# Kernel tuning notes

Measured on AMD Instinct MI355X. Metric: run time of the kernel, lower is better.

The kernel has to match this reference:

```python
import jax, jax.numpy as jnp
import numpy as np

B, N, E, H = 2, 4096, 512, 8
D = E // H  # head size


def setup_inputs() -> dict:
    key = jax.random.key(0)
    ks = jax.random.split(key, 11)
    s = 1.0 / np.sqrt(E)
    inp = {
        'q': jax.random.normal(ks[0], (B, N, E), jnp.float32),
        'k': jax.random.normal(ks[1], (B, N, E), jnp.float32),
        'v': jax.random.normal(ks[2], (B, N, E), jnp.float32),
        'Wq': jax.random.uniform(ks[3], (E, E), jnp.float32, -s, s),
        'bq': jax.random.uniform(ks[4], (E,), jnp.float32, -s, s),
        'Wk': jax.random.uniform(ks[5], (E, E), jnp.float32, -s, s),
        'bk': jax.random.uniform(ks[6], (E,), jnp.float32, -s, s),
        'Wv': jax.random.uniform(ks[7], (E, E), jnp.float32, -s, s),
        'bv': jax.random.uniform(ks[8], (E,), jnp.float32, -s, s),
        'Wo': jax.random.uniform(ks[9], (E, E), jnp.float32, -s, s),
        'bo': jax.random.uniform(ks[10], (E,), jnp.float32, -s, s),
    }
    return inp


def reference(q, k, v, Wq, bq, Wk, bk, Wv, bv, Wo, bo):
    # Linear projections (torch Linear: x @ W.T + b)
    qp = (q @ Wq.T + bq).reshape(B, N, H, D).transpose(0, 2, 1, 3)  # [B,H,N,D]
    kp = (k @ Wk.T + bk).reshape(B, N, H, D).transpose(0, 2, 1, 3)
    vp = (v @ Wv.T + bv).reshape(B, N, H, D).transpose(0, 2, 1, 3)
    scores = jnp.einsum('bhnd,bhmd->bhnm', qp, kp) / jnp.sqrt(jnp.float32(D))
    attn = jax.nn.softmax(scores, axis=-1)
    out = jnp.einsum('bhnm,bhmd->bhnd', attn, vp)  # [B,H,N,D]
    out = out.transpose(0, 2, 1, 3).reshape(B, N, E)
    return out @ Wo.T + bo
```

## Files before the change

kernel.cpp:

```cpp
#include <hip/hip_runtime.h>
#include <hip/hip_bf16.h>
#include <cstddef>
#include <cstdint>


typedef __bf16 bf16_t;
typedef __bf16 bf16x8 __attribute__((ext_vector_type(8)));
typedef __bf16 bf16x4 __attribute__((ext_vector_type(4)));
typedef float  f32x4  __attribute__((ext_vector_type(4)));

#define MFMA_BF16 __builtin_amdgcn_mfma_f32_16x16x32_bf16

static __device__ __forceinline__ bf16x8 cvt2(const float4& a, const float4& b) {
  return bf16x8{(bf16_t)a.x,(bf16_t)a.y,(bf16_t)a.z,(bf16_t)a.w,
                (bf16_t)b.x,(bf16_t)b.y,(bf16_t)b.z,(bf16_t)b.w};
}

static __device__ __forceinline__ uint32_t pk2(float a, float b) {
  uint32_t r;
  asm("v_cvt_pk_bf16_f32 %0, %1, %2" : "=v"(r) : "v"(a), "v"(b));
  return r;
}

__global__ void __launch_bounds__(256)
cvt_bf16(const float* __restrict__ q, const float* __restrict__ k,
         const float* __restrict__ v, const float* __restrict__ Wq,
         const float* __restrict__ Wk, const float* __restrict__ Wv,
         const float* __restrict__ Wo,
         bf16_t* __restrict__ qb, bf16_t* __restrict__ kb,
         bf16_t* __restrict__ vb, bf16_t* __restrict__ wq,
         bf16_t* __restrict__ wk, bf16_t* __restrict__ wv,
         bf16_t* __restrict__ wo)
{
  const int CQ = 524288;
  const int CW = 32768;
  const int TOT = 3 * CQ + 4 * CW;
  const int STRIDE = 2048 * 256;
  for (int c = blockIdx.x * 256 + threadIdx.x; c < TOT; c += STRIDE) {
    const float* src; bf16_t* dst; int off;
    if (c < 3 * CQ) {
      const int t = c >> 19;
      const int r = c & (CQ - 1);
      src = (t == 0) ? q : (t == 1) ? k : v;
      dst = (t == 0) ? qb : (t == 1) ? kb : vb;
      off = r << 3;
    } else {
      const int c2 = c - 3 * CQ;
      const int t = c2 >> 15;
      const int r = c2 & (CW - 1);
      src = (t == 0) ? Wq : (t == 1) ? Wk : (t == 2) ? Wv : Wo;
      dst = (t == 0) ? wq : (t == 1) ? wk : (t == 2) ? wv : wo;
      off = r << 3;
    }
    const float4 a = *(const float4*)(src + off);
    const float4 b = *(const float4*)(src + off + 4);
    *(bf16x8*)(dst + off) = cvt2(a, b);
  }
}

__global__ void __launch_bounds__(256, 3)
qkv_proj(const bf16_t* __restrict__ qb, const bf16_t* __restrict__ kb,
         const bf16_t* __restrict__ vb,
         const bf16_t* __restrict__ Wqb, const float* __restrict__ bq,
         const bf16_t* __restrict__ Wkb, const float* __restrict__ bk,
         const bf16_t* __restrict__ Wvb, const float* __restrict__ bv,
         bf16_t* __restrict__ Qp, bf16_t* __restrict__ Kp,
         bf16_t* __restrict__ Vt, float qscale)
{
  __shared__ __align__(16) bf16_t S[2 * 128 * 72];
  bf16_t* As = S;
  bf16_t* Bs = S + 128 * 72;

  const int l     = blockIdx.x;
  const int slice = l >> 8;
  const int inner = l & 255;
  const int mtile = ((inner >> 5) << 3) | (inner & 7);
  const int ntile = (inner >> 3) & 3;
  const int tid   = threadIdx.x;
  const int w     = tid >> 6;
  const int lane  = tid & 63;
  const int lr    = lane & 15;
  const int quad  = lane >> 4;
  const int wm    = w & 1;
  const int wn    = w >> 1;
  const int xrow  = tid >> 1, xcol = (tid & 1) << 5;

  const bf16_t* Xb   = (slice == 0) ? qb  : (slice == 1) ? kb  : vb;
  const bf16_t* W    = (slice == 0) ? Wqb : (slice == 1) ? Wkb : Wvb;
  const float*  bias = (slice == 0) ? bq  : (slice == 1) ? bk  : bv;
  const float scale  = (slice == 0) ? qscale : 1.0f;

  float bvv[4];
#pragma unroll
  for (int ci = 0; ci < 4; ++ci) bvv[ci] = bias[ntile * 128 + wn * 64 + ci * 16 + lr];

  f32x4 acc[4][4] = {};
  bf16x8 xa[4], wa[4];

#pragma unroll
  for (int j = 0; j < 4; ++j) {
    xa[j] = *(const bf16x8*)(Xb + (size_t)(mtile * 128 + xrow) * 512 + xcol + j * 8);
    wa[j] = *(const bf16x8*)(W  + (size_t)(ntile * 128 + xrow) * 512 + xcol + j * 8);
  }
#pragma unroll
  for (int j = 0; j < 4; ++j) {
    *(bf16x8*)(&As[xrow * 72 + xcol + j * 8]) = xa[j];
    *(bf16x8*)(&Bs[xrow * 72 + xcol + j * 8]) = wa[j];
  }
  __syncthreads();

  for (int it = 0; it < 8; ++it) {
    if (it != 7) {
      const int k0 = (it + 1) << 6;
#pragma unroll
      for (int j = 0; j < 4; ++j) {
        xa[j] = *(const bf16x8*)(Xb + (size_t)(mtile * 128 + xrow) * 512 + k0 + xcol + j * 8);
        wa[j] = *(const bf16x8*)(W  + (size_t)(ntile * 128 + xrow) * 512 + k0 + xcol + j * 8);
      }
    }
    bf16x8 af[4][2], bfr[4][2];
#pragma unroll
    for (int mi = 0; mi < 4; ++mi)
#pragma unroll
      for (int kh = 0; kh < 2; ++kh)
        af[mi][kh] = *(const bf16x8*)(&As[(wm * 64 + mi * 16 + lr) * 72 + (kh * 4 + quad) * 8]);
#pragma unroll
    for (int ci = 0; ci < 4; ++ci)
#pragma unroll
      for (int kh = 0; kh < 2; ++kh)
        bfr[ci][kh] = *(const bf16x8*)(&Bs[(wn * 64 + ci * 16 + lr) * 72 + (kh * 4 + quad) * 8]);
#pragma unroll
    for (int mi = 0; mi < 4; ++mi)
#pragma unroll
      for (int ci = 0; ci < 4; ++ci) {
        acc[mi][ci] = MFMA_BF16(af[mi][0], bfr[ci][0], acc[mi][ci], 0, 0, 0);
        acc[mi][ci] = MFMA_BF16(af[mi][1], bfr[ci][1], acc[mi][ci], 0, 0, 0);
      }
    __syncthreads();
    if (it != 7) {
#pragma unroll
      for (int j = 0; j < 4; ++j) {
        *(bf16x8*)(&As[xrow * 72 + xcol + j * 8]) = xa[j];
        *(bf16x8*)(&Bs[xrow * 72 + xcol + j * 8]) = wa[j];
      }
      __syncthreads();
    }
  }

  bf16_t (*Ct)[136] = (bf16_t (*)[136])S;
  if (slice < 2) {
    bf16_t* outQK = (slice == 0) ? Qp : Kp;
#pragma unroll
    for (int mi = 0; mi < 4; ++mi)
#pragma unroll
      for (int ci = 0; ci < 4; ++ci)
#pragma unroll
        for (int r = 0; r < 4; ++r)
          Ct[wm * 64 + mi * 16 + quad * 4 + r][wn * 64 + ci * 16 + lr] =
              (bf16_t)((acc[mi][ci][r] + bvv[ci]) * scale);
    __syncthreads();
    const int r2 = tid >> 1, half = tid & 1;
    const int gm = mtile * 128 + r2;
    const int b = gm >> 12, n = gm & 4095;
    const int gc0 = ntile * 128 + half * 64;
    const int h = gc0 >> 6;
    bf16_t* dst = outQK + (size_t)((b * 8 + h) * 4096 + n) * 64;
#pragma unroll
    for (int j = 0; j < 8; ++j)
      *(bf16x8*)(dst + j * 8) = *(const bf16x8*)(&Ct[r2][half * 64 + j * 8]);
  } else {
#pragma unroll
    for (int mi = 0; mi < 4; ++mi)
#pragma unroll
      for (int ci = 0; ci < 4; ++ci)
#pragma unroll
        for (int r = 0; r < 4; ++r)
          Ct[wn * 64 + ci * 16 + lr][wm * 64 + mi * 16 + quad * 4 + r] =
              (bf16_t)(acc[mi][ci][r] + bvv[ci]);
    __syncthreads();
    const int dline = tid >> 1, half = tid & 1;
    const int gc = ntile * 128 + dline;
    const int h = gc >> 6, dd = gc & 63;
    const int b = (mtile * 128) >> 12;
    const int n0 = (mtile * 128) & 4095;
    bf16_t* dst = Vt + (size_t)((b * 8 + h) * 64 + dd) * 4096 + n0 + half * 64;
#pragma unroll
    for (int j = 0; j < 8; ++j)
      *(bf16x8*)(dst + j * 8) = *(const bf16x8*)(&Ct[dline][half * 64 + j * 8]);
  }
}

__global__ void __launch_bounds__(256, 4)
o_proj(const bf16_t* __restrict__ Xb, const bf16_t* __restrict__ W,
       const float* __restrict__ bias, float* __restrict__ out)
{
  __shared__ __align__(16) bf16_t As[64 * 72];
  __shared__ __align__(16) bf16_t Bs[64 * 72];
  const int l     = blockIdx.x;
  const int mtile = l >> 3;
  const int ntile = l & 7;
  const int tid   = threadIdx.x;
  const int w     = tid >> 6;
  const int lane  = tid & 63;
  const int lr    = lane & 15;
  const int quad  = lane >> 4;
  const int wm    = w & 1;
  const int wn    = w >> 1;
  const int xrow  = tid >> 2, xcol = (tid & 3) << 4;

  float bvv[2];
#pragma unroll
  for (int ci = 0; ci < 2; ++ci) bvv[ci] = bias[ntile * 64 + wn * 32 + ci * 16 + lr];

  f32x4 acc[2][2] = {};
  bf16x8 xb[2], wb[2];

#pragma unroll
  for (int j = 0; j < 2; ++j) {
    xb[j] = *(const bf16x8*)(Xb + (size_t)(mtile * 64 + xrow) * 512 + xcol + j * 8);
    wb[j] = *(const bf16x8*)(W  + (size_t)(ntile * 64 + xrow) * 512 + xcol + j * 8);
  }
#pragma unroll
  for (int j = 0; j < 2; ++j) {
    *(bf16x8*)(&As[xrow * 72 + xcol + j * 8]) = xb[j];
    *(bf16x8*)(&Bs[xrow * 72 + xcol + j * 8]) = wb[j];
  }
  __syncthreads();

  for (int it = 0; it < 8; ++it) {
    if (it != 7) {
      const int k0 = (it + 1) << 6;
#pragma unroll
      for (int j = 0; j < 2; ++j) {
        xb[j] = *(const bf16x8*)(Xb + (size_t)(mtile * 64 + xrow) * 512 + k0 + xcol + j * 8);
        wb[j] = *(const bf16x8*)(W  + (size_t)(ntile * 64 + xrow) * 512 + k0 + xcol + j * 8);
      }
    }
    bf16x8 af[2][2], bfr[2][2];
#pragma unroll
    for (int mi = 0; mi < 2; ++mi)
#pragma unroll
      for (int kh = 0; kh < 2; ++kh)
        af[mi][kh] = *(const bf16x8*)(&As[(wm * 32 + mi * 16 + lr) * 72 + (kh * 4 + quad) * 8]);
#pragma unroll
    for (int ci = 0; ci < 2; ++ci)
#pragma unroll
      for (int kh = 0; kh < 2; ++kh)
        bfr[ci][kh] = *(const bf16x8*)(&Bs[(wn * 32 + ci * 16 + lr) * 72 + (kh * 4 + quad) * 8]);
#pragma unroll
    for (int mi = 0; mi < 2; ++mi)
#pragma unroll
      for (int ci = 0; ci < 2; ++ci) {
        acc[mi][ci] = MFMA_BF16(af[mi][0], bfr[ci][0], acc[mi][ci], 0, 0, 0);
        acc[mi][ci] = MFMA_BF16(af[mi][1], bfr[ci][1], acc[mi][ci], 0, 0, 0);
      }
    __syncthreads();
    if (it != 7) {
#pragma unroll
      for (int j = 0; j < 2; ++j) {
        *(bf16x8*)(&As[xrow * 72 + xcol + j * 8]) = xb[j];
        *(bf16x8*)(&Bs[xrow * 72 + xcol + j * 8]) = wb[j];
      }
      __syncthreads();
    }
  }

#pragma unroll
  for (int mi = 0; mi < 2; ++mi) {
    const int gm0 = mtile * 64 + wm * 32 + mi * 16 + quad * 4;
#pragma unroll
    for (int ci = 0; ci < 2; ++ci) {
      const int gc = ntile * 64 + wn * 32 + ci * 16 + lr;
#pragma unroll
      for (int r = 0; r < 4; ++r)
        out[(size_t)(gm0 + r) * 512 + gc] = acc[mi][ci][r] + bvv[ci];
    }
  }
}

__global__ void __launch_bounds__(256, 2)
flash_attn(const bf16_t* __restrict__ Qp, const bf16_t* __restrict__ Kp,
           const bf16_t* __restrict__ Vt, bf16_t* __restrict__ Oc)
{
  __shared__ __align__(16) bf16_t Klds[2][64 * 72];
  __shared__ __align__(16) bf16_t Vlds[2][64 * 72];

  const int tid  = threadIdx.x;
  const int w    = tid >> 6;
  const int lane = tid & 63, lr = lane & 15, quad = lane >> 4;
  const int bh   = blockIdx.x;
  const int qt0  = blockIdx.y * 128 + w * 32;

  const bf16_t* Qh = Qp + (size_t)bh * 4096 * 64;
  const bf16_t* Kh = Kp + (size_t)bh * 4096 * 64;
  const bf16_t* Vh = Vt + (size_t)bh * 64 * 4096;

  const int srow = w * 16 + (lane >> 2);
  const int scol = (lane & 3) << 4;

  bf16x8 qf[2][2];
#pragma unroll
  for (int qi = 0; qi < 2; ++qi)
#pragma unroll
    for (int kh = 0; kh < 2; ++kh)
      qf[qi][kh] = *(const bf16x8*)(Qh + (size_t)(qt0 + qi * 16 + lr) * 64 + kh * 32 + quad * 8);

  bf16x8 kst[2], vst[2];
#pragma unroll
  for (int j = 0; j < 2; ++j) {
    kst[j] = *(const bf16x8*)(Kh + (size_t)srow * 64 + scol + j * 8);
    vst[j] = *(const bf16x8*)(Vh + (size_t)srow * 4096 + scol + j * 8);
  }
#pragma unroll
  for (int j = 0; j < 2; ++j) {
    *(bf16x8*)(&Klds[0][srow * 72 + scol + j * 8]) = kst[j];
    *(bf16x8*)(&Vlds[0][srow * 72 + scol + j * 8]) = vst[j];
  }
  __syncthreads();

  f32x4 acc[2][4] = {};
  float lsum[2] = {0.f, 0.f};
  const f32x4 zero = {0.f, 0.f, 0.f, 0.f};

  for (int it = 0; it < 64; ++it) {
    const int cur = it & 1, nxt = cur ^ 1;

    if (it != 63) {
      const int kvn = (it + 1) << 6;
#pragma unroll
      for (int j = 0; j < 2; ++j) {
        kst[j] = *(const bf16x8*)(Kh + (size_t)(kvn + srow) * 64 + scol + j * 8);
        vst[j] = *(const bf16x8*)(Vh + (size_t)srow * 4096 + kvn + scol + j * 8);
      }
    }

    bf16x8 kf[4][2];
#pragma unroll
    for (int mt = 0; mt < 4; ++mt)
#pragma unroll
      for (int kh = 0; kh < 2; ++kh)
        kf[mt][kh] = *(const bf16x8*)(&Klds[cur][(mt * 16 + lr) * 72 + (kh * 4 + quad) * 8]);
    bf16x8 vf[4][2];
#pragma unroll
    for (int t = 0; t < 4; ++t)
#pragma unroll
      for (int kvh = 0; kvh < 2; ++kvh)
        vf[t][kvh] = *(const bf16x8*)(&Vlds[cur][(t * 16 + lr) * 72 + (kvh * 4 + quad) * 8]);

    f32x4 sT[4][2];
#pragma unroll
    for (int mt = 0; mt < 4; ++mt)
#pragma unroll
      for (int qi = 0; qi < 2; ++qi) {
        sT[mt][qi] = MFMA_BF16(kf[mt][0], qf[qi][0], zero, 0, 0, 0);
        sT[mt][qi] = MFMA_BF16(kf[mt][1], qf[qi][1], sT[mt][qi], 0, 0, 0);
      }

    bf16x8 pa[2][2];
#pragma unroll
    for (int qi = 0; qi < 2; ++qi) {
      uint32_t ap[4], bp[4];
#pragma unroll
      for (int mt = 0; mt < 4; ++mt) {
        float p0 = __builtin_amdgcn_exp2f(sT[mt][qi][0]);
        float p1 = __builtin_amdgcn_exp2f(sT[mt][qi][1]);
        float p2 = __builtin_amdgcn_exp2f(sT[mt][qi][2]);
        float p3 = __builtin_amdgcn_exp2f(sT[mt][qi][3]);
        lsum[qi] += (p0 + p1) + (p2 + p3);
        ap[mt] = pk2(p0, p1);
        bp[mt] = pk2(p2, p3);
      }
#pragma unroll
      for (int kvh = 0; kvh < 2; ++kvh) {
        uint32_t xa_ = ap[2 * kvh], ya_ = ap[2 * kvh + 1];
        asm("v_permlane32_swap_b32 %0, %1" : "+v"(xa_), "+v"(ya_));
        asm("v_permlane16_swap_b32 %0, %1" : "+v"(xa_), "+v"(ya_));
        uint32_t xb_ = bp[2 * kvh], yb_ = bp[2 * kvh + 1];
        asm("v_permlane32_swap_b32 %0, %1" : "+v"(xb_), "+v"(yb_));
        asm("v_permlane16_swap_b32 %0, %1" : "+v"(xb_), "+v"(yb_));
        union { uint32_t u[4]; bf16x8 v; } pu;
        pu.u[0] = xa_; pu.u[1] = xb_; pu.u[2] = ya_; pu.u[3] = yb_;
        pa[qi][kvh] = pu.v;
      }
    }

#pragma unroll
    for (int t = 0; t < 4; ++t)
#pragma unroll
      for (int qi = 0; qi < 2; ++qi) {
        acc[qi][t] = MFMA_BF16(pa[qi][0], vf[t][0], acc[qi][t], 0, 0, 0);
        acc[qi][t] = MFMA_BF16(pa[qi][1], vf[t][1], acc[qi][t], 0, 0, 0);
      }

    if (it != 63) {
#pragma unroll
      for (int j = 0; j < 2; ++j) {
        *(bf16x8*)(&Klds[nxt][srow * 72 + scol + j * 8]) = kst[j];
        *(bf16x8*)(&Vlds[nxt][srow * 72 + scol + j * 8]) = vst[j];
      }
    }
    __syncthreads();
  }

#pragma unroll
  for (int qi = 0; qi < 2; ++qi) {
    lsum[qi] += __shfl_xor(lsum[qi], 16);
    lsum[qi] += __shfl_xor(lsum[qi], 32);
  }

  const int b = bh >> 3, h = bh & 7;
  bf16_t* Ob = Oc + (size_t)b * 4096 * 512 + h * 64;
#pragma unroll
  for (int qi = 0; qi < 2; ++qi) {
    float inv[4];
#pragma unroll
    for (int r = 0; r < 4; ++r)
      inv[r] = 1.0f / __shfl(lsum[qi], quad * 4 + r);
#pragma unroll
    for (int t = 0; t < 4; ++t)
#pragma unroll
      for (int r = 0; r < 4; ++r) {
        const int n = qt0 + qi * 16 + quad * 4 + r;
        Ob[(size_t)n * 512 + t * 16 + lr] = (bf16_t)(acc[qi][t][r] * inv[r]);
      }
  }
}

extern "C" void kernel_launch(void* const* d_in, const int* in_sizes, int n_in,
                              void* d_out, int out_size, void* d_ws, size_t ws_size,
                              hipStream_t stream)
{
  const float* q  = (const float*)d_in[0];
  const float* k  = (const float*)d_in[1];
  const float* v  = (const float*)d_in[2];
  const float* Wq = (const float*)d_in[3];
  const float* bq = (const float*)d_in[4];
  const float* Wk = (const float*)d_in[5];
  const float* bk = (const float*)d_in[6];
  const float* Wv = (const float*)d_in[7];
  const float* bv = (const float*)d_in[8];
  const float* Wo = (const float*)d_in[9];
  const float* bo = (const float*)d_in[10];

  const size_t HEAD_ELEMS = (size_t)2 * 8 * 4096 * 64;
  const size_t W_ELEMS    = (size_t)512 * 512;

  bf16_t* base = (bf16_t*)d_ws;
  bf16_t* qb  = base;
  bf16_t* kb  = qb + HEAD_ELEMS;
  bf16_t* vb  = kb + HEAD_ELEMS;
  bf16_t* Qp  = vb + HEAD_ELEMS;
  bf16_t* Kp  = Qp + HEAD_ELEMS;
  bf16_t* Vt  = Kp + HEAD_ELEMS;
  bf16_t* wqb = Vt + HEAD_ELEMS;
  bf16_t* wkb = wqb + W_ELEMS;
  bf16_t* wvb = wkb + W_ELEMS;
  bf16_t* wob = wvb + W_ELEMS;
  bf16_t* Oc  = qb;

  const float qscale = 0.125f * 1.44269504f;

  cvt_bf16<<<dim3(2048), 256, 0, stream>>>(q, k, v, Wq, Wk, Wv, Wo,
                                           qb, kb, vb, wqb, wkb, wvb, wob);
  qkv_proj<<<dim3(768), 256, 0, stream>>>(qb, kb, vb, wqb, bq, wkb, bk,
                                          wvb, bv, Qp, Kp, Vt, qscale);
  flash_attn<<<dim3(16, 32), 256, 0, stream>>>(Qp, Kp, Vt, Oc);
  o_proj<<<dim3(1024), 256, 0, stream>>>(Oc, wob, bo, (float*)d_out);
}
```

Baseline: 226.7 us.

## Give each attention wave 64 query rows with half-split KV processing

The flash attention kernel now runs 2 waves per block instead of 4, and each wave handles 64 query rows instead of 32. Each K/V fragment read from LDS is therefore reused across four query tiles, halving LDS read traffic per FLOP. The KV tile is processed in two 32-column halves to limit live score registers. In exchange, per-thread register use rises (launch bounds of 128,1), and each thread must stage twice as many global loads. Fewer waves per block may also reduce latency hiding.

```diff
diff --git a/kernel.cpp b/kernel.cpp
--- a/kernel.cpp
+++ b/kernel.cpp
@@ -278,7 +278,7 @@
   }
 }
 
-__global__ void __launch_bounds__(256, 2)
+__global__ void __launch_bounds__(128, 1)
 flash_attn(const bf16_t* __restrict__ Qp, const bf16_t* __restrict__ Kp,
            const bf16_t* __restrict__ Vt, bf16_t* __restrict__ Oc)
 {
@@ -289,37 +289,41 @@
   const int w    = tid >> 6;
   const int lane = tid & 63, lr = lane & 15, quad = lane >> 4;
   const int bh   = blockIdx.x;
-  const int qt0  = blockIdx.y * 128 + w * 32;
+  const int qt0  = blockIdx.y * 128 + w * 64;
 
   const bf16_t* Qh = Qp + (size_t)bh * 4096 * 64;
   const bf16_t* Kh = Kp + (size_t)bh * 4096 * 64;
   const bf16_t* Vh = Vt + (size_t)bh * 64 * 4096;
 
-  const int srow = w * 16 + (lane >> 2);
-  const int scol = (lane & 3) << 4;
-
-  bf16x8 qf[2][2];
-#pragma unroll
-  for (int qi = 0; qi < 2; ++qi)
+  const int srow = tid >> 2;
+  const int scol = (tid & 3) << 4;
+
+  bf16x8 qf[4][2];
+#pragma unroll
+  for (int qi = 0; qi < 4; ++qi)
 #pragma unroll
     for (int kh = 0; kh < 2; ++kh)
       qf[qi][kh] = *(const bf16x8*)(Qh + (size_t)(qt0 + qi * 16 + lr) * 64 + kh * 32 + quad * 8);
 
-  bf16x8 kst[2], vst[2];
-#pragma unroll
-  for (int j = 0; j < 2; ++j) {
-    kst[j] = *(const bf16x8*)(Kh + (size_t)srow * 64 + scol + j * 8);
-    vst[j] = *(const bf16x8*)(Vh + (size_t)srow * 4096 + scol + j * 8);
-  }
-#pragma unroll
-  for (int j = 0; j < 2; ++j) {
-    *(bf16x8*)(&Klds[0][srow * 72 + scol + j * 8]) = kst[j];
-    *(bf16x8*)(&Vlds[0][srow * 72 + scol + j * 8]) = vst[j];
-  }
+  bf16x8 kst[4], vst[4];
+#pragma unroll
+  for (int rr = 0; rr < 2; ++rr)
+#pragma unroll
+    for (int j = 0; j < 2; ++j) {
+      kst[rr * 2 + j] = *(const bf16x8*)(Kh + (size_t)(srow + rr * 32) * 64 + scol + j * 8);
+      vst[rr * 2 + j] = *(const bf16x8*)(Vh + (size_t)(srow + rr * 32) * 4096 + scol + j * 8);
+    }
+#pragma unroll
+  for (int rr = 0; rr < 2; ++rr)
+#pragma unroll
+    for (int j = 0; j < 2; ++j) {
+      *(bf16x8*)(&Klds[0][(srow + rr * 32) * 72 + scol + j * 8]) = kst[rr * 2 + j];
+      *(bf16x8*)(&Vlds[0][(srow + rr * 32) * 72 + scol + j * 8]) = vst[rr * 2 + j];
+    }
   __syncthreads();
 
-  f32x4 acc[2][4] = {};
-  float lsum[2] = {0.f, 0.f};
+  f32x4 acc[4][4] = {};
+  float lsum[4] = {0.f, 0.f, 0.f, 0.f};
   const f32x4 zero = {0.f, 0.f, 0.f, 0.f};
 
   for (int it = 0; it < 64; ++it) {
@@ -328,82 +332,89 @@
     if (it != 63) {
       const int kvn = (it + 1) << 6;
 #pragma unroll
-      for (int j = 0; j < 2; ++j) {
-        kst[j] = *(const bf16x8*)(Kh + (size_t)(kvn + srow) * 64 + scol + j * 8);
-        vst[j] = *(const bf16x8*)(Vh + (size_t)srow * 4096 + kvn + scol + j * 8);
-      }
-    }
-
-    bf16x8 kf[4][2];
-#pragma unroll
-    for (int mt = 0; mt < 4; ++mt)
-#pragma unroll
-      for (int kh = 0; kh < 2; ++kh)
-        kf[mt][kh] = *(const bf16x8*)(&Klds[cur][(mt * 16 + lr) * 72 + (kh * 4 + quad) * 8]);
-    bf16x8 vf[4][2];
-#pragma unroll
-    for (int t = 0; t < 4; ++t)
-#pragma unroll
-      for (int kvh = 0; kvh < 2; ++kvh)
-        vf[t][kvh] = *(const bf16x8*)(&Vlds[cur][(t * 16 + lr) * 72 + (kvh * 4 + quad) * 8]);
-
-    f32x4 sT[4][2];
-#pragma unroll
-    for (int mt = 0; mt < 4; ++mt)
-#pragma unroll
-      for (int qi = 0; qi < 2; ++qi) {
-        sT[mt][qi] = MFMA_BF16(kf[mt][0], qf[qi][0], zero, 0, 0, 0);
-        sT[mt][qi] = MFMA_BF16(kf[mt][1], qf[qi][1], sT[mt][qi], 0, 0, 0);
-      }
-
-    bf16x8 pa[2][2];
-#pragma unroll
-    for (int qi = 0; qi < 2; ++qi) {
-      uint32_t ap[4], bp[4];
-#pragma unroll
-      for (int mt = 0; mt < 4; ++mt) {
-        float p0 = __builtin_amdgcn_exp2f(sT[mt][qi][0]);
-        float p1 = __builtin_amdgcn_exp2f(sT[mt][qi][1]);
-        float p2 = __builtin_amdgcn_exp2f(sT[mt][qi][2]);
-        float p3 = __builtin_amdgcn_exp2f(sT[mt][qi][3]);
-        lsum[qi] += (p0 + p1) + (p2 + p3);
-        ap[mt] = pk2(p0, p1);
-        bp[mt] = pk2(p2, p3);
-      }
-#pragma unroll
-      for (int kvh = 0; kvh < 2; ++kvh) {
-        uint32_t xa_ = ap[2 * kvh], ya_ = ap[2 * kvh + 1];
+      for (int rr = 0; rr < 2; ++rr)
+#pragma unroll
+        for (int j = 0; j < 2; ++j) {
+          kst[rr * 2 + j] = *(const bf16x8*)(Kh + (size_t)(kvn + srow + rr * 32) * 64 + scol + j * 8);
+          vst[rr * 2 + j] = *(const bf16x8*)(Vh + (size_t)(srow + rr * 32) * 4096 + kvn + scol + j * 8);
+        }
+    }
+
+#pragma unroll
+    for (int half = 0; half < 2; ++half) {
+      bf16x8 kf[2][2];
+#pragma unroll
+      for (int mm = 0; mm < 2; ++mm)
+#pragma unroll
+        for (int kh = 0; kh < 2; ++kh)
+          kf[mm][kh] = *(const bf16x8*)(&Klds[cur][((half * 2 + mm) * 16 + lr) * 72 + (kh * 4 + quad) * 8]);
+
+      bf16x8 vf[4];
+#pragma unroll
+      for (int t = 0; t < 4; ++t)
+        vf[t] = *(const bf16x8*)(&Vlds[cur][(t * 16 + lr) * 72 + (half * 4 + quad) * 8]);
+
+      f32x4 sT[2][4];
+#pragma unroll
+      for (int mm = 0; mm < 2; ++mm)
+#pragma unroll
+        for (int qi = 0; qi < 4; ++qi) {
+          sT[mm][qi] = MFMA_BF16(kf[mm][0], qf[qi][0], zero, 0, 0, 0);
+          sT[mm][qi] = MFMA_BF16(kf[mm][1], qf[qi][1], sT[mm][qi], 0, 0, 0);
+        }
+
+      bf16x8 pa[4];
+#pragma unroll
+      for (int qi = 0; qi < 4; ++qi) {
+        uint32_t a0, a1, b0, b1;
+        {
+          float p0 = __builtin_amdgcn_exp2f(sT[0][qi][0]);
+          float p1 = __builtin_amdgcn_exp2f(sT[0][qi][1]);
+          float p2 = __builtin_amdgcn_exp2f(sT[0][qi][2]);
+          float p3 = __builtin_amdgcn_exp2f(sT[0][qi][3]);
+          lsum[qi] += (p0 + p1) + (p2 + p3);
+          a0 = pk2(p0, p1); b0 = pk2(p2, p3);
+        }
+        {
+          float p0 = __builtin_amdgcn_exp2f(sT[1][qi][0]);
+          float p1 = __builtin_amdgcn_exp2f(sT[1][qi][1]);
+          float p2 = __builtin_amdgcn_exp2f(sT[1][qi][2]);
+          float p3 = __builtin_amdgcn_exp2f(sT[1][qi][3]);
+          lsum[qi] += (p0 + p1) + (p2 + p3);
+          a1 = pk2(p0, p1); b1 = pk2(p2, p3);
+        }
+        uint32_t xa_ = a0, ya_ = a1;
         asm("v_permlane32_swap_b32 %0, %1" : "+v"(xa_), "+v"(ya_));
         asm("v_permlane16_swap_b32 %0, %1" : "+v"(xa_), "+v"(ya_));
-        uint32_t xb_ = bp[2 * kvh], yb_ = bp[2 * kvh + 1];
+        uint32_t xb_ = b0, yb_ = b1;
         asm("v_permlane32_swap_b32 %0, %1" : "+v"(xb_), "+v"(yb_));
         asm("v_permlane16_swap_b32 %0, %1" : "+v"(xb_), "+v"(yb_));
         union { uint32_t u[4]; bf16x8 v; } pu;
         pu.u[0] = xa_; pu.u[1] = xb_; pu.u[2] = ya_; pu.u[3] = yb_;
-        pa[qi][kvh] = pu.v;
-      }
-    }
-
-#pragma unroll
-    for (int t = 0; t < 4; ++t)
-#pragma unroll
-      for (int qi = 0; qi < 2; ++qi) {
-        acc[qi][t] = MFMA_BF16(pa[qi][0], vf[t][0], acc[qi][t], 0, 0, 0);
-        acc[qi][t] = MFMA_BF16(pa[qi][1], vf[t][1], acc[qi][t], 0, 0, 0);
-      }
+        pa[qi] = pu.v;
+      }
+
+#pragma unroll
+      for (int t = 0; t < 4; ++t)
+#pragma unroll
+        for (int qi = 0; qi < 4; ++qi)
+          acc[qi][t] = MFMA_BF16(pa[qi], vf[t], acc[qi][t], 0, 0, 0);
+    }
 
     if (it != 63) {
 #pragma unroll
-      for (int j = 0; j < 2; ++j) {
-        *(bf16x8*)(&Klds[nxt][srow * 72 + scol + j * 8]) = kst[j];
-        *(bf16x8*)(&Vlds[nxt][srow * 72 + scol + j * 8]) = vst[j];
-      }
+      for (int rr = 0; rr < 2; ++rr)
+#pragma unroll
+        for (int j = 0; j < 2; ++j) {
+          *(bf16x8*)(&Klds[nxt][(srow + rr * 32) * 72 + scol + j * 8]) = kst[rr * 2 + j];
+          *(bf16x8*)(&Vlds[nxt][(srow + rr * 32) * 72 + scol + j * 8]) = vst[rr * 2 + j];
+        }
     }
     __syncthreads();
   }
 
 #pragma unroll
-  for (int qi = 0; qi < 2; ++qi) {
+  for (int qi = 0; qi < 4; ++qi) {
     lsum[qi] += __shfl_xor(lsum[qi], 16);
     lsum[qi] += __shfl_xor(lsum[qi], 32);
   }
@@ -411,7 +422,7 @@
   const int b = bh >> 3, h = bh & 7;
   bf16_t* Ob = Oc + (size_t)b * 4096 * 512 + h * 64;
 #pragma unroll
-  for (int qi = 0; qi < 2; ++qi) {
+  for (int qi = 0; qi < 4; ++qi) {
     float inv[4];
 #pragma unroll
     for (int r = 0; r < 4; ++r)
@@ -464,6 +475,6 @@
                                            qb, kb, vb, wqb, wkb, wvb, wob);
   qkv_proj<<<dim3(768), 256, 0, stream>>>(qb, kb, vb, wqb, bq, wkb, bk,
                                           wvb, bv, Qp, Kp, Vt, qscale);
-  flash_attn<<<dim3(16, 32), 256, 0, stream>>>(Qp, Kp, Vt, Oc);
+  flash_attn<<<dim3(16, 32), 128, 0, stream>>>(Qp, Kp, Vt, Oc);
   o_proj<<<dim3(1024), 256, 0, stream>>>(Oc, wob, bo, (float*)d_out);
 }
```

New measurement: 246.2 us. +8.6%, slower.

## Split attention KV range across two wave groups and remap projection tile order

Applied to the files above, without the earlier changes.

The attention block grows to 512 threads. Two groups of four waves each process half of the key/value sequence for the same 128 query rows, with separate double-buffered LDS regions. After the loop, the partial accumulators and row sums are merged through LDS and the second group exits. This doubles the waves working per block on this 512-block grid, aiming for better latency hiding, at the cost of more LDS and a reduction step. Block-to-tile mappings in the QKV and output projection kernels are also permuted to change cache locality.

```diff
diff --git a/kernel.cpp b/kernel.cpp
--- a/kernel.cpp
+++ b/kernel.cpp
@@ -74,7 +74,7 @@
   const int l     = blockIdx.x;
   const int slice = l >> 8;
   const int inner = l & 255;
-  const int mtile = ((inner >> 5) << 3) | (inner & 7);
+  const int mtile = ((inner & 7) << 3) | (inner >> 5);
   const int ntile = (inner >> 3) & 3;
   const int tid   = threadIdx.x;
   const int w     = tid >> 6;
@@ -197,8 +197,8 @@
   __shared__ __align__(16) bf16_t As[64 * 72];
   __shared__ __align__(16) bf16_t Bs[64 * 72];
   const int l     = blockIdx.x;
-  const int mtile = l >> 3;
-  const int ntile = l & 7;
+  const int mtile = ((l & 7) << 4) | ((l >> 3) & 15);
+  const int ntile = l >> 7;
   const int tid   = threadIdx.x;
   const int w     = tid >> 6;
   const int lane  = tid & 63;
@@ -278,25 +278,29 @@
   }
 }
 
-__global__ void __launch_bounds__(256, 2)
+__global__ void __launch_bounds__(512, 2)
 flash_attn(const bf16_t* __restrict__ Qp, const bf16_t* __restrict__ Kp,
            const bf16_t* __restrict__ Vt, bf16_t* __restrict__ Oc)
 {
-  __shared__ __align__(16) bf16_t Klds[2][64 * 72];
-  __shared__ __align__(16) bf16_t Vlds[2][64 * 72];
+  __shared__ __align__(16) bf16_t Klds[2][2][64 * 72];
+  __shared__ __align__(16) bf16_t Vlds[2][2][64 * 72];
 
   const int tid  = threadIdx.x;
   const int w    = tid >> 6;
+  const int g    = w >> 2;
+  const int wl   = w & 3;
   const int lane = tid & 63, lr = lane & 15, quad = lane >> 4;
   const int bh   = blockIdx.x;
-  const int qt0  = blockIdx.y * 128 + w * 32;
+  const int qt0  = blockIdx.y * 128 + wl * 32;
 
   const bf16_t* Qh = Qp + (size_t)bh * 4096 * 64;
   const bf16_t* Kh = Kp + (size_t)bh * 4096 * 64;
   const bf16_t* Vh = Vt + (size_t)bh * 64 * 4096;
 
-  const int srow = w * 16 + (lane >> 2);
-  const int scol = (lane & 3) << 4;
+  const int tg   = tid & 255;
+  const int srow = tg >> 2;
+  const int scol = (tg & 3) << 4;
+  const int kvbase = g << 11;
 
   bf16x8 qf[2][2];
 #pragma unroll
@@ -308,13 +312,13 @@
   bf16x8 kst[2], vst[2];
 #pragma unroll
   for (int j = 0; j < 2; ++j) {
-    kst[j] = *(const bf16x8*)(Kh + (size_t)srow * 64 + scol + j * 8);
-    vst[j] = *(const bf16x8*)(Vh + (size_t)srow * 4096 + scol + j * 8);
+    kst[j] = *(const bf16x8*)(Kh + (size_t)(kvbase + srow) * 64 + scol + j * 8);
+    vst[j] = *(const bf16x8*)(Vh + (size_t)srow * 4096 + kvbase + scol + j * 8);
   }
 #pragma unroll
   for (int j = 0; j < 2; ++j) {
-    *(bf16x8*)(&Klds[0][srow * 72 + scol + j * 8]) = kst[j];
-    *(bf16x8*)(&Vlds[0][srow * 72 + scol + j * 8]) = vst[j];
+    *(bf16x8*)(&Klds[g][0][srow * 72 + scol + j * 8]) = kst[j];
+    *(bf16x8*)(&Vlds[g][0][srow * 72 + scol + j * 8]) = vst[j];
   }
   __syncthreads();
 
@@ -322,11 +326,11 @@
   float lsum[2] = {0.f, 0.f};
   const f32x4 zero = {0.f, 0.f, 0.f, 0.f};
 
-  for (int it = 0; it < 64; ++it) {
+  for (int it = 0; it < 32; ++it) {
     const int cur = it & 1, nxt = cur ^ 1;
 
-    if (it != 63) {
-      const int kvn = (it + 1) << 6;
+    if (it != 31) {
+      const int kvn = kvbase + ((it + 1) << 6);
 #pragma unroll
       for (int j = 0; j < 2; ++j) {
         kst[j] = *(const bf16x8*)(Kh + (size_t)(kvn + srow) * 64 + scol + j * 8);
@@ -339,13 +343,13 @@
     for (int mt = 0; mt < 4; ++mt)
 #pragma unroll
       for (int kh = 0; kh < 2; ++kh)
-        kf[mt][kh] = *(const bf16x8*)(&Klds[cur][(mt * 16 + lr) * 72 + (kh * 4 + quad) * 8]);
+        kf[mt][kh] = *(const bf16x8*)(&Klds[g][cur][(mt * 16 + lr) * 72 + (kh * 4 + quad) * 8]);
     bf16x8 vf[4][2];
 #pragma unroll
     for (int t = 0; t < 4; ++t)
 #pragma unroll
       for (int kvh = 0; kvh < 2; ++kvh)
-        vf[t][kvh] = *(const bf16x8*)(&Vlds[cur][(t * 16 + lr) * 72 + (kvh * 4 + quad) * 8]);
+        vf[t][kvh] = *(const bf16x8*)(&Vlds[g][cur][(t * 16 + lr) * 72 + (kvh * 4 + quad) * 8]);
 
     f32x4 sT[4][2];
 #pragma unroll
@@ -392,11 +396,11 @@
         acc[qi][t] = MFMA_BF16(pa[qi][1], vf[t][1], acc[qi][t], 0, 0, 0);
       }
 
-    if (it != 63) {
+    if (it != 31) {
 #pragma unroll
       for (int j = 0; j < 2; ++j) {
-        *(bf16x8*)(&Klds[nxt][srow * 72 + scol + j * 8]) = kst[j];
-        *(bf16x8*)(&Vlds[nxt][srow * 72 + scol + j * 8]) = vst[j];
+        *(bf16x8*)(&Klds[g][nxt][srow * 72 + scol + j * 8]) = kst[j];
+        *(bf16x8*)(&Vlds[g][nxt][srow * 72 + scol + j * 8]) = vst[j];
       }
     }
     __syncthreads();
@@ -406,6 +410,33 @@
   for (int qi = 0; qi < 2; ++qi) {
     lsum[qi] += __shfl_xor(lsum[qi], 16);
     lsum[qi] += __shfl_xor(lsum[qi], 32);
+  }
+
+  float* accM  = (float*)&Klds[0][0][0];
+  float* lsumM = accM + 4 * 64 * 32;
+  const int mslot = (wl * 64 + lane);
+  if (g == 1) {
+#pragma unroll
+    for (int qi = 0; qi < 2; ++qi) {
+      lsumM[mslot * 2 + qi] = lsum[qi];
+#pragma unroll
+      for (int t = 0; t < 4; ++t)
+#pragma unroll
+        for (int r = 0; r < 4; ++r)
+          accM[mslot * 32 + qi * 16 + t * 4 + r] = acc[qi][t][r];
+    }
+  }
+  __syncthreads();
+  if (g == 1) return;
+
+#pragma unroll
+  for (int qi = 0; qi < 2; ++qi) {
+    lsum[qi] += lsumM[mslot * 2 + qi];
+#pragma unroll
+    for (int t = 0; t < 4; ++t)
+#pragma unroll
+      for (int r = 0; r < 4; ++r)
+        acc[qi][t][r] += accM[mslot * 32 + qi * 16 + t * 4 + r];
   }
 
   const int b = bh >> 3, h = bh & 7;
@@ -464,6 +495,6 @@
                                            qb, kb, vb, wqb, wkb, wvb, wob);
   qkv_proj<<<dim3(768), 256, 0, stream>>>(qb, kb, vb, wqb, bq, wkb, bk,
                                           wvb, bv, Qp, Kp, Vt, qscale);
-  flash_attn<<<dim3(16, 32), 256, 0, stream>>>(Qp, Kp, Vt, Oc);
+  flash_attn<<<dim3(16, 32), 512, 0, stream>>>(Qp, Kp, Vt, Oc);
   o_proj<<<dim3(1024), 256, 0, stream>>>(Oc, wob, bo, (float*)d_out);
 }
```

New measurement: 219.7 us. -3.1%, faster.
